# Kernel tuning notes

Hardware: AMD Instinct MI355X
Metric: run time of the kernel (lower is better)

## Reference

```python
import jax, jax.numpy as jnp
import numpy as np

ANG_RES = 5
DISP_MIN = -4
DISP_MAX = 4


def setup_inputs() -> dict:
    key = jax.random.key(0)
    k1, k2, k3 = jax.random.split(key, 3)
    b, c, h, w = 2, 8, 256, 256
    feature_map = jax.random.normal(k1, (b, c, ANG_RES * ANG_RES, h, w), dtype=jnp.float32)
    # validity mask in (0,1): mean over angular channels stays well away from 0
    mask = jax.random.uniform(k2, (b, ANG_RES * ANG_RES, h, w), dtype=jnp.float32)
    # grouped 1x1 conv weight: torch shape [c_out, k*k, 1, 1] with groups=c_in -> [8, 25]
    weight = jax.random.normal(k3, (8, ANG_RES * ANG_RES), dtype=jnp.float32) * 0.1
    return {"feature_map": feature_map, "mask": mask, "weight": weight}


def reference(feature_map, mask, weight):
    ang, dmin, dmax = ANG_RES, DISP_MIN, DISP_MAX
    m = ang // 2
    b, c, uv, h, w = feature_map.shape
    bdr = m * dmax
    # ZeroPad2d on the two trailing spatial dims
    fm = jnp.pad(feature_map, ((0, 0), (0, 0), (0, 0), (bdr, bdr), (bdr, bdr)))
    hp, wp = h + 2 * bdr, w + 2 * bdr
    # rearrange 'b c (u v) h w -> b c (u h) (v w)' : macro-pixel image [b,c,ang*hp,ang*wp]
    big = (fm.reshape(b, c, ang, ang, hp, wp)
             .transpose(0, 1, 2, 4, 3, 5)
             .reshape(b, c, ang * hp, ang * wp))
    H, W = mask.shape[2], mask.shape[3]
    mask_avg = jnp.mean(mask, axis=1)[:, None]  # [b,1,H,W]
    k2n = ang * ang
    r = weight.shape[0] // c  # outputs per group (grouped 1x1 conv)
    Wg = weight.reshape(c, r, k2n)
    costs = []
    for disp in range(dmin, dmax + 1):
        crop = m * (disp - dmin)          # crop applied to the padded macro image
        D = hp - disp                     # per-disparity unfold dilation
        # Unfold(kernel=ang, dilation=D) on the cropped macro image == for each
        # angular tap (u,v) a static HxW slice at offset crop + u*D (all offsets static)
        slices = [big[:, :, crop + u * D: crop + u * D + H,
                         crop + v * D: crop + v * D + W]
                  for u in range(ang) for v in range(ang)]
        shifted = jnp.stack(slices, axis=2)           # [b, c, ang^2, H, W]
        mod = shifted * mask[:, None]                 # modulate each angular view
        # grouped 1x1 conv: group g of ang^2 channels -> r outputs
        cost_i = jnp.einsum('bckhw,crk->bcrhw', mod, Wg).reshape(b, c * r, H, W)
        # torch `//` on floats == floor division
        costs.append(jnp.floor(cost_i / mask_avg))
    return jnp.stack(costs, axis=2)  # [b, c_out, n_disp, H, W]
```

## Files before the change

kernel.cpp:

```cpp
#include <hip/hip_runtime.h>
#include <math.h>

#define HH 256
#define WW 256
#define CC 8
#define KK 25
#define ND 9
#define NB 2
#define HW (HH * WW)

typedef int int4v __attribute__((ext_vector_type(4)));

__device__ float llvm_amdgcn_raw_buffer_load_fp32(int4v srsrc, int voffset,
                                                  int soffset, int aux)
    __asm("llvm.amdgcn.raw.buffer.load.f32");

__global__ __launch_bounds__(256, 4) void cost_kernel(
    const float* __restrict__ fm,
    const float* __restrict__ mask,
    const float* __restrict__ wgt,
    float* __restrict__ out)
{
#pragma clang fp contract(off)
    const int j = threadIdx.x;

    const int vb = blockIdx.x;
    const int nid = (vb & 7) * (NB * CC * HH / 8) + (vb >> 3);
    const int i = nid & 255;
    const int c = (nid >> 8) & 7;
    const int b = nid >> 11;

    const float* fmb = fm + (size_t)(b * CC + c) * KK * HW;
    const float* mb  = mask + (size_t)b * KK * HW + (size_t)i * WW + j;
    const float* wc  = wgt + c * KK;

    int voff[17];
#pragma unroll
    for (int s = 0; s < 17; ++s) voff[s] = (j + (s - 8)) * 4;

    float acc[ND];
#pragma unroll
    for (int dd = 0; dd < ND; ++dd) acc[dd] = 0.f;
    float msum = 0.f;

    for (int g = 0; g < 5; ++g) {
        const int du = g - 2;
#pragma unroll
        for (int v = 0; v < 5; ++v) {
            const int k  = 5 * g + v;
            const int dv = v - 2;
            const float mk = mb[(size_t)k * HW];
            const float wk = wc[k];
            const float* fpk = fmb + (size_t)k * HW;

            float f[ND];
#pragma unroll
            for (int dd = 0; dd < ND; ++dd) {
                const int d  = dd - 4;
                const int y  = i - du * d;
                const int yv = ((unsigned)y < HH);
                const int yc = min(max(y, 0), HH - 1);
                const float* rowp = fpk + yc * WW;
                int4v srd;
                srd.x = (int)(uintptr_t)rowp;
                srd.y = (int)((uintptr_t)rowp >> 32);
                srd.z = yv ? (WW * 4) : 0;
                srd.w = 0x00020000;
                const int s = 8 - dv * d;
                f[dd] = llvm_amdgcn_raw_buffer_load_fp32(srd, voff[s], 0, 0);
            }
            msum = __fadd_rn(msum, mk);
#pragma unroll
            for (int dd = 0; dd < ND; ++dd) {
                const float p = __fmul_rn(f[dd], mk);
                const float t = __fmul_rn(p, wk);
                acc[dd] = __fadd_rn(acc[dd], t);
            }
        }
    }

    const float mavg = __fdiv_rn(msum, 25.0f);
    float* ob = out + (size_t)(b * CC + c) * ND * HW + (size_t)i * WW + j;
#pragma unroll
    for (int dd = 0; dd < ND; ++dd)
        ob[(size_t)dd * HW] = floorf(__fdiv_rn(acc[dd], mavg));
}

extern "C" void kernel_launch(void* const* d_in, const int* in_sizes, int n_in,
                              void* d_out, int out_size, void* d_ws, size_t ws_size,
                              hipStream_t stream) {
    const float* fm   = (const float*)d_in[0];
    const float* mask = (const float*)d_in[1];
    const float* wgt  = (const float*)d_in[2];
    float* out = (float*)d_out;

    dim3 grid(NB * CC * HH);
    dim3 block(WW);
    cost_kernel<<<grid, block, 0, stream>>>(fm, mask, wgt, out);
}
```

Before: 53.37 us.

## Give each thread two pixels and split disparities across block halves

Each thread now computes two adjacent columns, and the block is split so one half handles disparities 0-4 and the other 5-8. Loads of feature values, mask and output use 2-wide vector accesses where the shift is even, falling back to two scalar loads when it is odd. This aims to cut load instruction count and raise bytes per memory op. In exchange the mask loads and sums are duplicated across the two halves, and the two halves run different disparity counts, so their work is unbalanced. The launch_bounds occupancy hint is also dropped.

```diff
diff --git a/kernel.cpp b/kernel.cpp
--- a/kernel.cpp
+++ b/kernel.cpp
@@ -9,39 +9,29 @@
 #define NB 2
 #define HW (HH * WW)
 
-typedef int int4v __attribute__((ext_vector_type(4)));
+typedef int   int4v   __attribute__((ext_vector_type(4)));
+typedef float float2v __attribute__((ext_vector_type(2)));
 
 __device__ float llvm_amdgcn_raw_buffer_load_fp32(int4v srsrc, int voffset,
                                                   int soffset, int aux)
     __asm("llvm.amdgcn.raw.buffer.load.f32");
+__device__ float2v llvm_amdgcn_raw_buffer_load_v2fp32(int4v srsrc, int voffset,
+                                                      int soffset, int aux)
+    __asm("llvm.amdgcn.raw.buffer.load.v2f32");
 
-__global__ __launch_bounds__(256, 4) void cost_kernel(
-    const float* __restrict__ fm,
-    const float* __restrict__ mask,
-    const float* __restrict__ wgt,
-    float* __restrict__ out)
+template<int HALF>
+__device__ __forceinline__ void compute_half(
+    int i, int jj, const float* __restrict__ fmb, const float* __restrict__ mb,
+    const float* __restrict__ wc, float* __restrict__ ob)
 {
-#pragma clang fp contract(off)
-    const int j = threadIdx.x;
+    constexpr int DD0 = HALF ? 5 : 0;
+    constexpr int NDD = HALF ? 4 : 5;
+    const int jj4 = jj * 4;
 
-    const int vb = blockIdx.x;
-    const int nid = (vb & 7) * (NB * CC * HH / 8) + (vb >> 3);
-    const int i = nid & 255;
-    const int c = (nid >> 8) & 7;
-    const int b = nid >> 11;
-
-    const float* fmb = fm + (size_t)(b * CC + c) * KK * HW;
-    const float* mb  = mask + (size_t)b * KK * HW + (size_t)i * WW + j;
-    const float* wc  = wgt + c * KK;
-
-    int voff[17];
+    float acc0[NDD], acc1[NDD];
 #pragma unroll
-    for (int s = 0; s < 17; ++s) voff[s] = (j + (s - 8)) * 4;
-
-    float acc[ND];
-#pragma unroll
-    for (int dd = 0; dd < ND; ++dd) acc[dd] = 0.f;
-    float msum = 0.f;
+    for (int q = 0; q < NDD; ++q) { acc0[q] = 0.f; acc1[q] = 0.f; }
+    float ms0 = 0.f, ms1 = 0.f;
 
     for (int g = 0; g < 5; ++g) {
         const int du = g - 2;
@@ -49,14 +39,14 @@
         for (int v = 0; v < 5; ++v) {
             const int k  = 5 * g + v;
             const int dv = v - 2;
-            const float mk = mb[(size_t)k * HW];
+            const float2v mk = *(const float2v*)(mb + (size_t)k * HW);
             const float wk = wc[k];
             const float* fpk = fmb + (size_t)k * HW;
 
-            float f[ND];
+            float fx[NDD], fy[NDD];
 #pragma unroll
-            for (int dd = 0; dd < ND; ++dd) {
-                const int d  = dd - 4;
+            for (int q = 0; q < NDD; ++q) {
+                const int d  = DD0 + q - 4;
                 const int y  = i - du * d;
                 const int yv = ((unsigned)y < HH);
                 const int yc = min(max(y, 0), HH - 1);
@@ -66,24 +56,67 @@
                 srd.y = (int)((uintptr_t)rowp >> 32);
                 srd.z = yv ? (WW * 4) : 0;
                 srd.w = 0x00020000;
-                const int s = 8 - dv * d;
-                f[dd] = llvm_amdgcn_raw_buffer_load_fp32(srd, voff[s], 0, 0);
+                const int sp = -dv * d;
+                const int vo = jj4 + sp * 4;
+                if ((sp & 1) == 0) {
+                    const float2v t =
+                        llvm_amdgcn_raw_buffer_load_v2fp32(srd, vo, 0, 0);
+                    fx[q] = t.x; fy[q] = t.y;
+                } else {
+                    fx[q] = llvm_amdgcn_raw_buffer_load_fp32(srd, vo, 0, 0);
+                    fy[q] = llvm_amdgcn_raw_buffer_load_fp32(srd, vo + 4, 0, 0);
+                }
             }
-            msum = __fadd_rn(msum, mk);
+            ms0 = __fadd_rn(ms0, mk.x);
+            ms1 = __fadd_rn(ms1, mk.y);
 #pragma unroll
-            for (int dd = 0; dd < ND; ++dd) {
-                const float p = __fmul_rn(f[dd], mk);
-                const float t = __fmul_rn(p, wk);
-                acc[dd] = __fadd_rn(acc[dd], t);
+            for (int q = 0; q < NDD; ++q) {
+                const float p0 = __fmul_rn(fx[q], mk.x);
+                const float t0 = __fmul_rn(p0, wk);
+                acc0[q] = __fadd_rn(acc0[q], t0);
+                const float p1 = __fmul_rn(fy[q], mk.y);
+                const float t1 = __fmul_rn(p1, wk);
+                acc1[q] = __fadd_rn(acc1[q], t1);
             }
         }
     }
 
-    const float mavg = __fdiv_rn(msum, 25.0f);
-    float* ob = out + (size_t)(b * CC + c) * ND * HW + (size_t)i * WW + j;
+    const float mavg0 = __fdiv_rn(ms0, 25.0f);
+    const float mavg1 = __fdiv_rn(ms1, 25.0f);
 #pragma unroll
-    for (int dd = 0; dd < ND; ++dd)
-        ob[(size_t)dd * HW] = floorf(__fdiv_rn(acc[dd], mavg));
+    for (int q = 0; q < NDD; ++q) {
+        const int dd = DD0 + q;
+        float2v o;
+        o.x = floorf(__fdiv_rn(acc0[q], mavg0));
+        o.y = floorf(__fdiv_rn(acc1[q], mavg1));
+        *(float2v*)(ob + (size_t)dd * HW) = o;
+    }
+}
+
+__global__ __launch_bounds__(256) void cost_kernel(
+    const float* __restrict__ fm,
+    const float* __restrict__ mask,
+    const float* __restrict__ wgt,
+    float* __restrict__ out)
+{
+#pragma clang fp contract(off)
+    const int tid  = threadIdx.x;
+    const int half = tid >> 7;
+    const int jj   = (tid & 127) << 1;
+
+    const int vb = blockIdx.x;
+    const int nid = (vb & 7) * (NB * CC * HH / 8) + (vb >> 3);
+    const int i = nid & 255;
+    const int c = (nid >> 8) & 7;
+    const int b = nid >> 11;
+
+    const float* fmb = fm + (size_t)(b * CC + c) * KK * HW;
+    const float* mb  = mask + (size_t)b * KK * HW + (size_t)i * WW + jj;
+    const float* wc  = wgt + c * KK;
+    float* ob = out + (size_t)(b * CC + c) * ND * HW + (size_t)i * WW + jj;
+
+    if (half == 0) compute_half<0>(i, jj, fmb, mb, wc, ob);
+    else           compute_half<1>(i, jj, fmb, mb, wc, ob);
 }
 
 extern "C" void kernel_launch(void* const* d_in, const int* in_sizes, int n_in,
@@ -95,6 +128,6 @@
     float* out = (float*)d_out;
 
     dim3 grid(NB * CC * HH);
-    dim3 block(WW);
+    dim3 block(256);
     cost_kernel<<<grid, block, 0, stream>>>(fm, mask, wgt, out);
 }
```

After: 78.68 us. +47.4%, slower.
